# Kernel optimization log

Measured on AMD Instinct MI355X. Metric: run time of the kernel, lower is better.

## Reference

```python
import jax, jax.numpy as jnp
import numpy as np

T = 20000          # document length in tokens
EMBED_DIM = 300    # GloVe 840B.300d
STATE_DIM = 400    # 2 * lstm_dim (bidirectional)
HIDDEN = 150       # Scorer hidden_dim default
MAX_N = 10         # span widths 1..10
G_DIM = 2 * STATE_DIM + EMBED_DIM  # 1100


def _mlp3(x, W1, b1, W2, b2, W3, b3):
    # Scorer: Linear -> ReLU -> Linear -> ReLU -> Linear(->1)
    h = jax.nn.relu(x @ W1 + b1)
    h = jax.nn.relu(h @ W2 + b2)
    return h @ W3 + b3


def _span_features(embeds, states, attn_logits):
    """Vectorized SpanEncoder: for every window of width n in 1..MAX_N,
    softmax the per-token attention logits within the window, attention-pool
    the word embeddings, and concat [state_start, state_end, pooled].
    Returns g of shape [sum_n (T-n+1), G_DIM]."""
    gs = []
    for n in range(1, MAX_N + 1):
        S = T - n + 1  # number of width-n spans
        # [n, S] windowed logits and [n, S, E] windowed embeds via shifted slices
        a = jnp.stack([attn_logits[j:j + S] for j in range(n)], axis=0)
        w = jax.nn.softmax(a, axis=0)  # softmax within each span (dim=0 in torch)
        we = jnp.stack([embeds[j:j + S] for j in range(n)], axis=0)
        pooled = jnp.einsum('ns,nse->se', w, we)  # [S, E]
        g = jnp.concatenate([states[:S], states[n - 1:n - 1 + S], pooled], axis=-1)
        gs.append(g)
    return jnp.concatenate(gs, axis=0)


def setup_inputs() -> dict:
    key = jax.random.key(0)
    ks = jax.random.split(key, 16)
    sc = 0.05
    return {
        'embeds': jax.random.normal(ks[0], (T, EMBED_DIM), jnp.float32),
        'states': jax.random.normal(ks[1], (T, STATE_DIM), jnp.float32),
        'attn_W1': jax.random.normal(ks[2], (STATE_DIM, HIDDEN), jnp.float32) * sc,
        'attn_b1': jnp.zeros((HIDDEN,), jnp.float32),
        'attn_W2': jax.random.normal(ks[3], (HIDDEN, HIDDEN), jnp.float32) * sc,
        'attn_b2': jnp.zeros((HIDDEN,), jnp.float32),
        'attn_W3': jax.random.normal(ks[4], (HIDDEN, 1), jnp.float32) * sc,
        'attn_b3': jnp.zeros((1,), jnp.float32),
        'sc_W1': jax.random.normal(ks[5], (G_DIM, HIDDEN), jnp.float32) * sc,
        'sc_b1': jnp.zeros((HIDDEN,), jnp.float32),
        'sc_W2': jax.random.normal(ks[6], (HIDDEN, HIDDEN), jnp.float32) * sc,
        'sc_b2': jnp.zeros((HIDDEN,), jnp.float32),
        'sc_W3': jax.random.normal(ks[7], (HIDDEN, 1), jnp.float32) * sc,
        'sc_b3': jnp.zeros((1,), jnp.float32),
    }


def reference(embeds, states, attn_W1, attn_b1, attn_W2, attn_b2, attn_W3, attn_b3,
              sc_W1, sc_b1, sc_W2, sc_b2, sc_W3, sc_b3):
    # SpanAttention: per-token scalar attention logit from the BiLSTM state
    attn_logits = _mlp3(states, attn_W1, attn_b1, attn_W2, attn_b2, attn_W3, attn_b3)[:, 0]
    # SpanEncoder: ragged windowed attention pooling + boundary-state concat
    g = _span_features(embeds, states, attn_logits)  # [10T-45, 1100]
    # SpanScorer: MLP score per span
    scores = _mlp3(g, sc_W1, sc_b1, sc_W2, sc_b2, sc_W3, sc_b3)[:, 0]
    return scores
```

## Files before the change

### kernel.cpp

```cpp
#include <hip/hip_runtime.h>
#include <hip/hip_bf16.h>
#include <math.h>

#define T_LEN 20000
#define HID 150

typedef __attribute__((ext_vector_type(8))) __bf16 bf16x8;
typedef __attribute__((ext_vector_type(4))) float f32x4;

__device__ __forceinline__ short f2bf(float f) {
    unsigned u = __float_as_uint(f);
    u = (u + 0x7fff + ((u >> 16) & 1)) >> 16;
    return (short)u;
}

__device__ __forceinline__ unsigned pk2(float a, float b) {
    __hip_bfloat162 h = __float22bfloat162_rn(make_float2(a, b));
    return *(unsigned*)&h;
}

__device__ __forceinline__ bf16x8 cvt8(float4 a, float4 b) {
    union { unsigned u[4]; bf16x8 v; } r;
    r.u[0] = pk2(a.x, a.y);
    r.u[1] = pk2(a.z, a.w);
    r.u[2] = pk2(b.x, b.y);
    r.u[3] = pk2(b.z, b.w);
    return r.v;
}

__device__ __forceinline__ float2 ubf2(unsigned u) {
    return make_float2(__uint_as_float(u << 16),
                       __uint_as_float(u & 0xffff0000u));
}

__global__ __launch_bounds__(256) void wprep(
    const float* __restrict__ sc_W1, const float* __restrict__ attn_W1,
    const float* __restrict__ attn_W2, const float* __restrict__ sc_W2,
    short* __restrict__ frag)
{
    int t = blockIdx.x * 256 + threadIdx.x;
    if (t >= 302080) return;
    float v = 0.f;
    if (t < 199680) {
        int e = t & 7, g = t >> 3;
        int lane = g & 63, h = g >> 6;
        int ks = h % 13, nt = h / 13;
        int k = ks * 32 + (lane >> 4) * 8 + e;
        int cs = (nt % 10) * 16 + (lane & 15);
        if (k < 400 && cs < HID) {
            if (nt < 10)      v = sc_W1[(long)k * HID + cs];
            else if (nt < 20) v = sc_W1[(long)(400 + k) * HID + cs];
            else              v = attn_W1[(long)k * HID + cs];
        }
    } else if (t < 250880) {
        int r = t - 199680;
        int e = r & 7, g = r >> 3;
        int lane = g & 63, h = g >> 6;
        int ks = h % 10, nt = h / 10;
        int k = ks * 32 + (lane >> 4) * 8 + e;
        int cs = nt * 16 + (lane & 15);
        if (k < 300 && cs < HID) v = sc_W1[(long)(800 + k) * HID + cs];
    } else if (t < 276480) {
        int r = t - 250880;
        int e = r & 7, g = r >> 3;
        int lane = g & 63, h = g >> 6;
        int ks = h % 5, nt = h / 5;
        int k = ks * 32 + (lane >> 4) * 8 + e;
        int cs = nt * 16 + (lane & 15);
        if (k < HID && cs < HID) v = attn_W2[(long)k * HID + cs];
    } else {
        int r = t - 276480;
        int e = r & 7, g = r >> 3;
        int lane = g & 63, h = g >> 6;
        int ks = h % 5, nt = h / 5;
        int k = ks * 32 + (lane >> 4) * 8 + e;
        int cs = nt * 16 + (lane & 15);
        if (k < HID && cs < HID) v = sc_W2[(long)k * HID + cs];
    }
    frag[t] = f2bf(v);
}

template<int NT, int KS>
__device__ __forceinline__ void mm_tiles(
    const short* __restrict__ fb,
    const short* As,
    int w, int lane, f32x4* acc)
{
    #pragma unroll
    for (int ks = 0; ks < KS; ++ks) {
        bf16x8 af = *(const bf16x8*)&As[(ks * 64 + lane) * 8];
        bf16x8 bfr[NT];
        #pragma unroll
        for (int t = 0; t < NT; ++t)
            bfr[t] = *(const bf16x8*)&fb[((4 * t + w) * KS + ks) << 9];
        #pragma unroll
        for (int t = 0; t < NT; ++t)
            acc[t] = __builtin_amdgcn_mfma_f32_16x16x32_bf16(bfr[t], af, acc[t], 0, 0, 0);
    }
}

__global__ __launch_bounds__(256, 4) void fusedAP(
    const float* __restrict__ states, const float* __restrict__ embeds,
    const short* __restrict__ frag,
    const float* __restrict__ scb1, const float* __restrict__ ab1,
    const float* __restrict__ ab2, const float* __restrict__ aW3,
    const float* __restrict__ ab3,
    short* __restrict__ Ubf, short* __restrict__ Vbf, short* __restrict__ Pbf,
    float* __restrict__ logits)
{
    __shared__ short As[13 * 64 * 8];
    __shared__ short h1s[16 * 168];
    __shared__ float red[16][4];
    __shared__ float sb1[160], ab1s[160];
    const int tid = threadIdx.x;
    const int w = tid >> 6, lane = tid & 63;
    const int ml = lane & 15, kg = lane >> 4;
    const int m0 = blockIdx.x * 16;

    for (int t = tid; t < 160; t += 256) {
        sb1[t]  = (t < HID) ? scb1[t] : 0.f;
        ab1s[t] = (t < HID) ? ab1[t]  : 0.f;
    }
    for (int g = tid; g < 13 * 64; g += 256) {
        int ks = g >> 6, l2 = g & 63;
        int k = ks * 32 + ((l2 >> 4) << 3);
        const float* Ar = states + (long)(m0 + (l2 & 15)) * 400;
        float4 a0 = make_float4(0.f, 0.f, 0.f, 0.f), a1 = a0;
        if (k + 4 <= 400) a0 = *(const float4*)&Ar[k];
        if (k + 8 <= 400) a1 = *(const float4*)&Ar[k + 4];
        *(bf16x8*)&As[g * 8] = cvt8(a0, a1);
    }
    __syncthreads();

    f32x4 acc[8];
    #pragma unroll
    for (int t = 0; t < 8; ++t) acc[t] = (f32x4){0.f, 0.f, 0.f, 0.f};
    const short* fb = frag + lane * 8;
    if (w < 2) mm_tiles<8, 13>(fb, As, w, lane, acc);
    else       mm_tiles<7, 13>(fb, As, w, lane, acc);

    const int nT = (w < 2) ? 8 : 7;
    #pragma unroll
    for (int t = 0; t < 8; ++t) {
        if (t < nT) {
            int nt = 4 * t + w;
            if (nt < 10) {
                int col0 = nt * 16 + kg * 4;
                float v[4];
                #pragma unroll
                for (int r = 0; r < 4; ++r) {
                    int c = col0 + r;
                    v[r] = (c < HID) ? acc[t][r] + sb1[c] : 0.f;
                }
                *(uint2*)&Ubf[(long)(m0 + ml) * 160 + col0] =
                    make_uint2(pk2(v[0], v[1]), pk2(v[2], v[3]));
            } else if (nt < 20) {
                int col0 = (nt - 10) * 16 + kg * 4;
                float v[4];
                #pragma unroll
                for (int r = 0; r < 4; ++r) {
                    int c = col0 + r;
                    v[r] = (c < HID) ? acc[t][r] : 0.f;
                }
                *(uint2*)&Vbf[(long)(m0 + ml) * 160 + col0] =
                    make_uint2(pk2(v[0], v[1]), pk2(v[2], v[3]));
            } else {
                int col0 = (nt - 20) * 16 + kg * 4;
                float v[4];
                #pragma unroll
                for (int r = 0; r < 4; ++r) {
                    int c = col0 + r;
                    v[r] = (c < HID) ? fmaxf(acc[t][r] + ab1s[c], 0.f) : 0.f;
                }
                *(uint2*)&h1s[ml * 168 + col0] =
                    make_uint2(pk2(v[0], v[1]), pk2(v[2], v[3]));
            }
        }
    }
    __syncthreads();

    for (int g = tid; g < 10 * 64; g += 256) {
        int ks = g >> 6, l2 = g & 63;
        int k = ks * 32 + ((l2 >> 4) << 3);
        const float* Er = embeds + (long)(m0 + (l2 & 15)) * 300;
        float4 a0 = make_float4(0.f, 0.f, 0.f, 0.f), a1 = a0;
        if (k + 4 <= 300) a0 = *(const float4*)&Er[k];
        if (k + 8 <= 300) a1 = *(const float4*)&Er[k + 4];
        *(bf16x8*)&As[g * 8] = cvt8(a0, a1);
    }
    __syncthreads();

    {
        f32x4 accP[3];
        #pragma unroll
        for (int t = 0; t < 3; ++t) accP[t] = (f32x4){0.f, 0.f, 0.f, 0.f};
        const short* fP = frag + 199680 + lane * 8;
        if (w < 2) mm_tiles<3, 10>(fP, As, w, lane, accP);
        else       mm_tiles<2, 10>(fP, As, w, lane, accP);

        const int nTp = (w < 2) ? 3 : 2;
        #pragma unroll
        for (int t = 0; t < 3; ++t) {
            if (t < nTp) {
                int nt = 4 * t + w;
                int col0 = nt * 16 + kg * 4;
                float v[4];
                #pragma unroll
                for (int r = 0; r < 4; ++r) {
                    int c = col0 + r;
                    v[r] = (c < HID) ? accP[t][r] : 0.f;
                }
                *(uint2*)&Pbf[(long)(m0 + ml) * 160 + col0] =
                    make_uint2(pk2(v[0], v[1]), pk2(v[2], v[3]));
            }
        }
    }

    const short* fAt2 = frag + 250880 + lane * 8;
    bf16x8 af2[5];
    #pragma unroll
    for (int ks = 0; ks < 5; ++ks)
        af2[ks] = *(const bf16x8*)&h1s[ml * 168 + ks * 32 + kg * 8];

    const int nT2 = (w < 2) ? 3 : 2;
    float score[4] = {0.f, 0.f, 0.f, 0.f};
    #pragma unroll
    for (int t = 0; t < 3; ++t) {
        if (t < nT2) {
            int nt = 4 * t + w;
            bf16x8 wb[5];
            #pragma unroll
            for (int ks = 0; ks < 5; ++ks)
                wb[ks] = *(const bf16x8*)&fAt2[(nt * 5 + ks) << 9];
            f32x4 a2 = {0.f, 0.f, 0.f, 0.f};
            #pragma unroll
            for (int ks = 0; ks < 5; ++ks)
                a2 = __builtin_amdgcn_mfma_f32_16x16x32_bf16(af2[ks], wb[ks], a2, 0, 0, 0);
            int col = nt * 16 + ml;
            float b2v = (col < HID) ? ab2[col] : 0.f;
            float w3v = (col < HID) ? aW3[col] : 0.f;
            #pragma unroll
            for (int r = 0; r < 4; ++r)
                score[r] += fmaxf(a2[r] + b2v, 0.f) * w3v;
        }
    }
    #pragma unroll
    for (int r = 0; r < 4; ++r) {
        score[r] += __shfl_xor(score[r], 1);
        score[r] += __shfl_xor(score[r], 2);
        score[r] += __shfl_xor(score[r], 4);
        score[r] += __shfl_xor(score[r], 8);
    }
    if (ml == 0) {
        #pragma unroll
        for (int r = 0; r < 4; ++r) red[kg * 4 + r][w] = score[r];
    }
    __syncthreads();
    if (tid < 16)
        logits[m0 + tid] = red[tid][0] + red[tid][1] + red[tid][2] + red[tid][3] + ab3[0];
}

__global__ __launch_bounds__(256) void span_all(
    const short* __restrict__ Ubf, const short* __restrict__ Vbf,
    const short* __restrict__ Pbf, const float* __restrict__ logits,
    const short* __restrict__ fW2, const float* __restrict__ b2,
    const float* __restrict__ W3, const float* __restrict__ b3,
    float* __restrict__ out)
{
    __shared__ short h1s[2][32 * 168];
    __shared__ float red[2][32][2];
    __shared__ float Ls[48], ebuf[48];
    __shared__ float b2s[160], W3s[160];

    const int tid = threadIdx.x;
    const int s0 = blockIdx.x * 32;
    const int nlo = blockIdx.y ? 6 : 1;
    const int nhi = blockIdx.y ? 10 : 5;

    if (tid < 48) {
        int r = s0 + tid; if (r > T_LEN - 1) r = T_LEN - 1;
        Ls[tid] = (tid < 41) ? logits[r] : -1e30f;
    }
    for (int t = tid; t < 160; t += 256) {
        b2s[t] = (t < HID) ? b2[t] : 0.f;
        W3s[t] = (t < HID) ? W3[t] : 0.f;
    }
    __syncthreads();
    if (tid < 48) {
        float M = -1e30f;
        for (int t = 0; t < 41; ++t) M = fmaxf(M, Ls[t]);
        ebuf[tid] = (tid < 41) ? expf(Ls[tid] - M) : 0.f;
    }
    __syncthreads();

    const int i = tid >> 3;
    const int q = tid & 7;
    const int d0 = 20 * q;
    const int s = s0 + i;
    int su = s; if (su > T_LEN - 1) su = T_LEN - 1;

    float Ur[20];
    {
        const uint2* U2 = (const uint2*)&Ubf[(long)su * 160 + d0];
        #pragma unroll
        for (int c = 0; c < 5; ++c) {
            uint2 uv = U2[c];
            float2 a = ubf2(uv.x), b_ = ubf2(uv.y);
            Ur[4 * c + 0] = a.x;  Ur[4 * c + 1] = a.y;
            Ur[4 * c + 2] = b_.x; Ur[4 * c + 3] = b_.y;
        }
    }
    float accp[20];
    #pragma unroll
    for (int d = 0; d < 20; ++d) accp[d] = 0.f;
    float den = 0.f;

    for (int j = 0; j < nlo - 1; ++j) {
        int rr_ = s + j; if (rr_ > T_LEN - 1) rr_ = T_LEN - 1;
        float e = ebuf[i + j];
        den += e;
        const uint2* P2 = (const uint2*)&Pbf[(long)rr_ * 160 + d0];
        #pragma unroll
        for (int c = 0; c < 5; ++c) {
            uint2 pv = P2[c];
            float2 a = ubf2(pv.x), b_ = ubf2(pv.y);
            accp[4 * c + 0] += e * a.x;  accp[4 * c + 1] += e * a.y;
            accp[4 * c + 2] += e * b_.x; accp[4 * c + 3] += e * b_.y;
        }
    }

    const int w = tid >> 6, lane = tid & 63;
    const int ml = lane & 15, kg = lane >> 4;
    const int mt = w >> 1;
    const int nt0 = (w & 1) * 5;
    const float bb = b3[0];
    const short* fw = fW2 + ((nt0 * 5) << 9) + lane * 8;

    auto phase1 = [&](int n, int p) {
        int rr_ = s + n - 1; if (rr_ > T_LEN - 1) rr_ = T_LEN - 1;
        float e = ebuf[i + n - 1];
        den += e;
        {
            const uint2* P2 = (const uint2*)&Pbf[(long)rr_ * 160 + d0];
            #pragma unroll
            for (int c = 0; c < 5; ++c) {
                uint2 pv = P2[c];
                float2 a = ubf2(pv.x), b_ = ubf2(pv.y);
                accp[4 * c + 0] += e * a.x;  accp[4 * c + 1] += e * a.y;
                accp[4 * c + 2] += e * b_.x; accp[4 * c + 3] += e * b_.y;
            }
        }
        float invd = 1.f / den;
        {
            const uint2* V2 = (const uint2*)&Vbf[(long)rr_ * 160 + d0];
            #pragma unroll
            for (int c = 0; c < 5; ++c) {
                uint2 vv = V2[c];
                float2 a = ubf2(vv.x), b_ = ubf2(vv.y);
                float x0 = fmaxf(Ur[4 * c + 0] + a.x  + accp[4 * c + 0] * invd, 0.f);
                float x1 = fmaxf(Ur[4 * c + 1] + a.y  + accp[4 * c + 1] * invd, 0.f);
                float x2 = fmaxf(Ur[4 * c + 2] + b_.x + accp[4 * c + 2] * invd, 0.f);
                float x3 = fmaxf(Ur[4 * c + 3] + b_.y + accp[4 * c + 3] * invd, 0.f);
                *(uint2*)&h1s[p][i * 168 + d0 + 4 * c] =
                    make_uint2(pk2(x0, x1), pk2(x2, x3));
            }
        }
    };

    phase1(nlo, 0);
    __syncthreads();

    for (int n = nlo; n <= nhi; ++n) {
        const int p = (n - nlo) & 1;

        bf16x8 af[5];
        #pragma unroll
        for (int ks = 0; ks < 5; ++ks)
            af[ks] = *(const bf16x8*)&h1s[p][(mt * 16 + ml) * 168 + ks * 32 + kg * 8];

        if (n < nhi) phase1(n + 1, 1 - p);

        bf16x8 wc[5], wn[5];
        #pragma unroll
        for (int ks = 0; ks < 5; ++ks)
            wc[ks] = *(const bf16x8*)&fw[ks << 9];

        float sc[4] = {0.f, 0.f, 0.f, 0.f};
        #pragma unroll
        for (int j = 0; j < 5; ++j) {
            if (j < 4) {
                #pragma unroll
                for (int ks = 0; ks < 5; ++ks)
                    wn[ks] = *(const bf16x8*)&fw[((j + 1) * 5 + ks) << 9];
            }
            f32x4 a2 = {0.f, 0.f, 0.f, 0.f};
            #pragma unroll
            for (int ks = 0; ks < 5; ++ks)
                a2 = __builtin_amdgcn_mfma_f32_16x16x32_bf16(af[ks], wc[ks], a2, 0, 0, 0);
            int col = (nt0 + j) * 16 + ml;
            float b2v = b2s[col], w3v = W3s[col];
            #pragma unroll
            for (int r = 0; r < 4; ++r)
                sc[r] += fmaxf(a2[r] + b2v, 0.f) * w3v;
            #pragma unroll
            for (int ks = 0; ks < 5; ++ks) wc[ks] = wn[ks];
        }
        #pragma unroll
        for (int r = 0; r < 4; ++r) {
            sc[r] += __shfl_xor(sc[r], 1);
            sc[r] += __shfl_xor(sc[r], 2);
            sc[r] += __shfl_xor(sc[r], 4);
            sc[r] += __shfl_xor(sc[r], 8);
        }
        if (ml == 0) {
            #pragma unroll
            for (int r = 0; r < 4; ++r)
                red[p][mt * 16 + kg * 4 + r][w & 1] = sc[r];
        }
        __syncthreads();
        if (tid < 32) {
            int S = T_LEN - n + 1;
            int off = (n - 1) * (T_LEN + 1) - (n - 1) * n / 2;
            int sr = s0 + tid;
            if (sr < S) out[off + sr] = red[p][tid][0] + red[p][tid][1] + bb;
        }
    }
}

extern "C" void kernel_launch(void* const* d_in, const int* in_sizes, int n_in,
                              void* d_out, int out_size, void* d_ws, size_t ws_size,
                              hipStream_t stream) {
    const float* embeds  = (const float*)d_in[0];
    const float* states  = (const float*)d_in[1];
    const float* attn_W1 = (const float*)d_in[2];
    const float* attn_b1 = (const float*)d_in[3];
    const float* attn_W2 = (const float*)d_in[4];
    const float* attn_b2 = (const float*)d_in[5];
    const float* attn_W3 = (const float*)d_in[6];
    const float* attn_b3 = (const float*)d_in[7];
    const float* sc_W1   = (const float*)d_in[8];
    const float* sc_b1   = (const float*)d_in[9];
    const float* sc_W2   = (const float*)d_in[10];
    const float* sc_b2   = (const float*)d_in[11];
    const float* sc_W3   = (const float*)d_in[12];
    const float* sc_b3   = (const float*)d_in[13];
    float* out = (float*)d_out;

    short* wsS = (short*)d_ws;
    short* Ubf = wsS;
    short* Vbf = wsS + 3200256;
    short* Pbf = wsS + 6400512;
    short* frag = wsS + 9600768;
    float* logits = (float*)(wsS + 9902848);

    wprep<<<1180, 256, 0, stream>>>(sc_W1, attn_W1, attn_W2, sc_W2, frag);
    fusedAP<<<1250, 256, 0, stream>>>(states, embeds, frag, sc_b1, attn_b1,
                                      attn_b2, attn_W3, attn_b3,
                                      Ubf, Vbf, Pbf, logits);
    span_all<<<dim3(625, 2), 256, 0, stream>>>(Ubf, Vbf, Pbf, logits,
                                               frag + 276480, sc_b2, sc_W3, sc_b3,
                                               out);
}
```

Before: 191.6 us.

## Process two row tiles per block in fusedAP and restructure span_all weight loads

fusedAP now handles 32 rows per block with 6 warps, and each warp owns 5 contiguous column tiles. Each B-fragment load from global memory feeds two MFMAs (one per 16-row group), and the next k-step's weights are software-prefetched, which halves grid size and weight traffic per row. In span_all, phase1 for the next width now runs before the A-fragment reads, and the register double-buffered weight prefetch is replaced by direct per-MFMA global loads, which lowers register pressure but may expose load latency. Larger LDS and register use per block may lower occupancy.

```diff
diff --git a/kernel.cpp b/kernel.cpp
--- a/kernel.cpp
+++ b/kernel.cpp
@@ -80,26 +80,7 @@
     frag[t] = f2bf(v);
 }
 
-template<int NT, int KS>
-__device__ __forceinline__ void mm_tiles(
-    const short* __restrict__ fb,
-    const short* As,
-    int w, int lane, f32x4* acc)
-{
-    #pragma unroll
-    for (int ks = 0; ks < KS; ++ks) {
-        bf16x8 af = *(const bf16x8*)&As[(ks * 64 + lane) * 8];
-        bf16x8 bfr[NT];
-        #pragma unroll
-        for (int t = 0; t < NT; ++t)
-            bfr[t] = *(const bf16x8*)&fb[((4 * t + w) * KS + ks) << 9];
-        #pragma unroll
-        for (int t = 0; t < NT; ++t)
-            acc[t] = __builtin_amdgcn_mfma_f32_16x16x32_bf16(bfr[t], af, acc[t], 0, 0, 0);
-    }
-}
-
-__global__ __launch_bounds__(256, 4) void fusedAP(
+__global__ __launch_bounds__(384, 3) void fusedAP(
     const float* __restrict__ states, const float* __restrict__ embeds,
     const short* __restrict__ frag,
     const float* __restrict__ scb1, const float* __restrict__ ab1,
@@ -108,61 +89,88 @@
     short* __restrict__ Ubf, short* __restrict__ Vbf, short* __restrict__ Pbf,
     float* __restrict__ logits)
 {
-    __shared__ short As[13 * 64 * 8];
-    __shared__ short h1s[16 * 168];
-    __shared__ float red[16][4];
+    __shared__ short As[2 * 13 * 64 * 8];
+    __shared__ short h1s[32 * 168];
+    __shared__ float red[32][6];
     __shared__ float sb1[160], ab1s[160];
     const int tid = threadIdx.x;
     const int w = tid >> 6, lane = tid & 63;
     const int ml = lane & 15, kg = lane >> 4;
-    const int m0 = blockIdx.x * 16;
-
-    for (int t = tid; t < 160; t += 256) {
+    const int m0 = blockIdx.x * 32;
+
+    for (int t = tid; t < 160; t += 384) {
         sb1[t]  = (t < HID) ? scb1[t] : 0.f;
         ab1s[t] = (t < HID) ? ab1[t]  : 0.f;
     }
-    for (int g = tid; g < 13 * 64; g += 256) {
-        int ks = g >> 6, l2 = g & 63;
+    for (int idx = tid; idx < 2 * 13 * 64; idx += 384) {
+        int g = idx / 832, r = idx - g * 832;
+        int ks = r >> 6, l2 = r & 63;
         int k = ks * 32 + ((l2 >> 4) << 3);
-        const float* Ar = states + (long)(m0 + (l2 & 15)) * 400;
+        const float* Ar = states + (long)(m0 + g * 16 + (l2 & 15)) * 400;
         float4 a0 = make_float4(0.f, 0.f, 0.f, 0.f), a1 = a0;
         if (k + 4 <= 400) a0 = *(const float4*)&Ar[k];
         if (k + 8 <= 400) a1 = *(const float4*)&Ar[k + 4];
-        *(bf16x8*)&As[g * 8] = cvt8(a0, a1);
-    }
-    __syncthreads();
-
-    f32x4 acc[8];
-    #pragma unroll
-    for (int t = 0; t < 8; ++t) acc[t] = (f32x4){0.f, 0.f, 0.f, 0.f};
+        *(bf16x8*)&As[idx * 8] = cvt8(a0, a1);
+    }
+    __syncthreads();
+
+    f32x4 acc[5][2];
+    #pragma unroll
+    for (int t = 0; t < 5; ++t)
+        #pragma unroll
+        for (int g = 0; g < 2; ++g)
+            acc[t][g] = (f32x4){0.f, 0.f, 0.f, 0.f};
+
     const short* fb = frag + lane * 8;
-    if (w < 2) mm_tiles<8, 13>(fb, As, w, lane, acc);
-    else       mm_tiles<7, 13>(fb, As, w, lane, acc);
-
-    const int nT = (w < 2) ? 8 : 7;
-    #pragma unroll
-    for (int t = 0; t < 8; ++t) {
-        if (t < nT) {
-            int nt = 4 * t + w;
-            if (nt < 10) {
+    const int t5 = w * 5;
+
+    bf16x8 bcur[5], bnxt[5];
+    #pragma unroll
+    for (int t = 0; t < 5; ++t)
+        bcur[t] = *(const bf16x8*)&fb[((t5 + t) * 13 + 0) << 9];
+
+    #pragma unroll
+    for (int ks = 0; ks < 13; ++ks) {
+        if (ks < 12) {
+            #pragma unroll
+            for (int t = 0; t < 5; ++t)
+                bnxt[t] = *(const bf16x8*)&fb[((t5 + t) * 13 + ks + 1) << 9];
+        }
+        bf16x8 af0 = *(const bf16x8*)&As[(ks * 64 + lane) * 8];
+        bf16x8 af1 = *(const bf16x8*)&As[((832 + ks * 64) + lane) * 8];
+        #pragma unroll
+        for (int t = 0; t < 5; ++t) {
+            acc[t][0] = __builtin_amdgcn_mfma_f32_16x16x32_bf16(bcur[t], af0, acc[t][0], 0, 0, 0);
+            acc[t][1] = __builtin_amdgcn_mfma_f32_16x16x32_bf16(bcur[t], af1, acc[t][1], 0, 0, 0);
+        }
+        #pragma unroll
+        for (int t = 0; t < 5; ++t) bcur[t] = bnxt[t];
+    }
+
+    #pragma unroll
+    for (int t = 0; t < 5; ++t) {
+        int nt = t5 + t;
+        #pragma unroll
+        for (int g = 0; g < 2; ++g) {
+            if (w < 2) {
                 int col0 = nt * 16 + kg * 4;
                 float v[4];
                 #pragma unroll
                 for (int r = 0; r < 4; ++r) {
                     int c = col0 + r;
-                    v[r] = (c < HID) ? acc[t][r] + sb1[c] : 0.f;
+                    v[r] = (c < HID) ? acc[t][g][r] + sb1[c] : 0.f;
                 }
-                *(uint2*)&Ubf[(long)(m0 + ml) * 160 + col0] =
+                *(uint2*)&Ubf[(long)(m0 + g * 16 + ml) * 160 + col0] =
                     make_uint2(pk2(v[0], v[1]), pk2(v[2], v[3]));
-            } else if (nt < 20) {
+            } else if (w < 4) {
                 int col0 = (nt - 10) * 16 + kg * 4;
                 float v[4];
                 #pragma unroll
                 for (int r = 0; r < 4; ++r) {
                     int c = col0 + r;
-                    v[r] = (c < HID) ? acc[t][r] : 0.f;
+                    v[r] = (c < HID) ? acc[t][g][r] : 0.f;
                 }
-                *(uint2*)&Vbf[(long)(m0 + ml) * 160 + col0] =
+                *(uint2*)&Vbf[(long)(m0 + g * 16 + ml) * 160 + col0] =
                     make_uint2(pk2(v[0], v[1]), pk2(v[2], v[3]));
             } else {
                 int col0 = (nt - 20) * 16 + kg * 4;
@@ -170,94 +178,142 @@
                 #pragma unroll
                 for (int r = 0; r < 4; ++r) {
                     int c = col0 + r;
-                    v[r] = (c < HID) ? fmaxf(acc[t][r] + ab1s[c], 0.f) : 0.f;
+                    v[r] = (c < HID) ? fmaxf(acc[t][g][r] + ab1s[c], 0.f) : 0.f;
                 }
-                *(uint2*)&h1s[ml * 168 + col0] =
+                *(uint2*)&h1s[(g * 16 + ml) * 168 + col0] =
                     make_uint2(pk2(v[0], v[1]), pk2(v[2], v[3]));
             }
         }
     }
     __syncthreads();
 
-    for (int g = tid; g < 10 * 64; g += 256) {
-        int ks = g >> 6, l2 = g & 63;
+    for (int idx = tid; idx < 2 * 10 * 64; idx += 384) {
+        int g = idx / 640, r = idx - g * 640;
+        int ks = r >> 6, l2 = r & 63;
         int k = ks * 32 + ((l2 >> 4) << 3);
-        const float* Er = embeds + (long)(m0 + (l2 & 15)) * 300;
+        const float* Er = embeds + (long)(m0 + g * 16 + (l2 & 15)) * 300;
         float4 a0 = make_float4(0.f, 0.f, 0.f, 0.f), a1 = a0;
         if (k + 4 <= 300) a0 = *(const float4*)&Er[k];
         if (k + 8 <= 300) a1 = *(const float4*)&Er[k + 4];
-        *(bf16x8*)&As[g * 8] = cvt8(a0, a1);
-    }
-    __syncthreads();
-
+        *(bf16x8*)&As[idx * 8] = cvt8(a0, a1);
+    }
+    __syncthreads();
+
+    const int tB = (w < 4) ? 2 * w : (w == 4 ? 8 : 9);
+    const int nTP = (w < 4) ? 2 : 1;
     {
-        f32x4 accP[3];
-        #pragma unroll
-        for (int t = 0; t < 3; ++t) accP[t] = (f32x4){0.f, 0.f, 0.f, 0.f};
+        f32x4 accP[2][2];
+        #pragma unroll
+        for (int t = 0; t < 2; ++t)
+            #pragma unroll
+            for (int g = 0; g < 2; ++g)
+                accP[t][g] = (f32x4){0.f, 0.f, 0.f, 0.f};
+
         const short* fP = frag + 199680 + lane * 8;
-        if (w < 2) mm_tiles<3, 10>(fP, As, w, lane, accP);
-        else       mm_tiles<2, 10>(fP, As, w, lane, accP);
-
-        const int nTp = (w < 2) ? 3 : 2;
-        #pragma unroll
-        for (int t = 0; t < 3; ++t) {
-            if (t < nTp) {
-                int nt = 4 * t + w;
-                int col0 = nt * 16 + kg * 4;
-                float v[4];
-                #pragma unroll
-                for (int r = 0; r < 4; ++r) {
-                    int c = col0 + r;
-                    v[r] = (c < HID) ? accP[t][r] : 0.f;
+        bf16x8 pcur[2], pnxt[2];
+        #pragma unroll
+        for (int t = 0; t < 2; ++t)
+            if (t < nTP) pcur[t] = *(const bf16x8*)&fP[((tB + t) * 10 + 0) << 9];
+
+        #pragma unroll
+        for (int ks = 0; ks < 10; ++ks) {
+            if (ks < 9) {
+                #pragma unroll
+                for (int t = 0; t < 2; ++t)
+                    if (t < nTP) pnxt[t] = *(const bf16x8*)&fP[((tB + t) * 10 + ks + 1) << 9];
+            }
+            bf16x8 af0 = *(const bf16x8*)&As[(ks * 64 + lane) * 8];
+            bf16x8 af1 = *(const bf16x8*)&As[((640 + ks * 64) + lane) * 8];
+            #pragma unroll
+            for (int t = 0; t < 2; ++t) {
+                if (t < nTP) {
+                    accP[t][0] = __builtin_amdgcn_mfma_f32_16x16x32_bf16(pcur[t], af0, accP[t][0], 0, 0, 0);
+                    accP[t][1] = __builtin_amdgcn_mfma_f32_16x16x32_bf16(pcur[t], af1, accP[t][1], 0, 0, 0);
                 }
-                *(uint2*)&Pbf[(long)(m0 + ml) * 160 + col0] =
-                    make_uint2(pk2(v[0], v[1]), pk2(v[2], v[3]));
+            }
+            #pragma unroll
+            for (int t = 0; t < 2; ++t) pcur[t] = pnxt[t];
+        }
+
+        #pragma unroll
+        for (int t = 0; t < 2; ++t) {
+            if (t < nTP) {
+                int col0 = (tB + t) * 16 + kg * 4;
+                #pragma unroll
+                for (int g = 0; g < 2; ++g) {
+                    float v[4];
+                    #pragma unroll
+                    for (int r = 0; r < 4; ++r) {
+                        int c = col0 + r;
+                        v[r] = (c < HID) ? accP[t][g][r] : 0.f;
+                    }
+                    *(uint2*)&Pbf[(long)(m0 + g * 16 + ml) * 160 + col0] =
+                        make_uint2(pk2(v[0], v[1]), pk2(v[2], v[3]));
+                }
             }
         }
     }
 
     const short* fAt2 = frag + 250880 + lane * 8;
-    bf16x8 af2[5];
-    #pragma unroll
-    for (int ks = 0; ks < 5; ++ks)
-        af2[ks] = *(const bf16x8*)&h1s[ml * 168 + ks * 32 + kg * 8];
-
-    const int nT2 = (w < 2) ? 3 : 2;
-    float score[4] = {0.f, 0.f, 0.f, 0.f};
-    #pragma unroll
-    for (int t = 0; t < 3; ++t) {
-        if (t < nT2) {
-            int nt = 4 * t + w;
+    bf16x8 af2[2][5];
+    #pragma unroll
+    for (int g = 0; g < 2; ++g)
+        #pragma unroll
+        for (int ks = 0; ks < 5; ++ks)
+            af2[g][ks] = *(const bf16x8*)&h1s[(g * 16 + ml) * 168 + ks * 32 + kg * 8];
+
+    float score[2][4];
+    #pragma unroll
+    for (int g = 0; g < 2; ++g)
+        #pragma unroll
+        for (int r = 0; r < 4; ++r) score[g][r] = 0.f;
+
+    #pragma unroll
+    for (int t = 0; t < 2; ++t) {
+        if (t < nTP) {
+            int nt = tB + t;
             bf16x8 wb[5];
             #pragma unroll
             for (int ks = 0; ks < 5; ++ks)
                 wb[ks] = *(const bf16x8*)&fAt2[(nt * 5 + ks) << 9];
-            f32x4 a2 = {0.f, 0.f, 0.f, 0.f};
-            #pragma unroll
-            for (int ks = 0; ks < 5; ++ks)
-                a2 = __builtin_amdgcn_mfma_f32_16x16x32_bf16(af2[ks], wb[ks], a2, 0, 0, 0);
+            f32x4 a2[2];
+            a2[0] = (f32x4){0.f, 0.f, 0.f, 0.f};
+            a2[1] = (f32x4){0.f, 0.f, 0.f, 0.f};
+            #pragma unroll
+            for (int g = 0; g < 2; ++g)
+                #pragma unroll
+                for (int ks = 0; ks < 5; ++ks)
+                    a2[g] = __builtin_amdgcn_mfma_f32_16x16x32_bf16(af2[g][ks], wb[ks], a2[g], 0, 0, 0);
             int col = nt * 16 + ml;
             float b2v = (col < HID) ? ab2[col] : 0.f;
             float w3v = (col < HID) ? aW3[col] : 0.f;
             #pragma unroll
+            for (int g = 0; g < 2; ++g)
+                #pragma unroll
+                for (int r = 0; r < 4; ++r)
+                    score[g][r] += fmaxf(a2[g][r] + b2v, 0.f) * w3v;
+        }
+    }
+    #pragma unroll
+    for (int g = 0; g < 2; ++g)
+        #pragma unroll
+        for (int r = 0; r < 4; ++r) {
+            score[g][r] += __shfl_xor(score[g][r], 1);
+            score[g][r] += __shfl_xor(score[g][r], 2);
+            score[g][r] += __shfl_xor(score[g][r], 4);
+            score[g][r] += __shfl_xor(score[g][r], 8);
+        }
+    if (ml == 0) {
+        #pragma unroll
+        for (int g = 0; g < 2; ++g)
+            #pragma unroll
             for (int r = 0; r < 4; ++r)
-                score[r] += fmaxf(a2[r] + b2v, 0.f) * w3v;
-        }
-    }
-    #pragma unroll
-    for (int r = 0; r < 4; ++r) {
-        score[r] += __shfl_xor(score[r], 1);
-        score[r] += __shfl_xor(score[r], 2);
-        score[r] += __shfl_xor(score[r], 4);
-        score[r] += __shfl_xor(score[r], 8);
-    }
-    if (ml == 0) {
-        #pragma unroll
-        for (int r = 0; r < 4; ++r) red[kg * 4 + r][w] = score[r];
-    }
-    __syncthreads();
-    if (tid < 16)
-        logits[m0 + tid] = red[tid][0] + red[tid][1] + red[tid][2] + red[tid][3] + ab3[0];
+                red[g * 16 + kg * 4 + r][w] = score[g][r];
+    }
+    __syncthreads();
+    if (tid < 32)
+        logits[m0 + tid] = red[tid][0] + red[tid][1] + red[tid][2] +
+                           red[tid][3] + red[tid][4] + red[tid][5] + ab3[0];
 }
 
 __global__ __launch_bounds__(256) void span_all(
@@ -334,7 +390,6 @@
     const int mt = w >> 1;
     const int nt0 = (w & 1) * 5;
     const float bb = b3[0];
-    const short* fw = fW2 + ((nt0 * 5) << 9) + lane * 8;
 
     auto phase1 = [&](int n, int p) {
         int rr_ = s + n - 1; if (rr_ > T_LEN - 1) rr_ = T_LEN - 1;
@@ -372,38 +427,28 @@
 
     for (int n = nlo; n <= nhi; ++n) {
         const int p = (n - nlo) & 1;
+        if (n < nhi) phase1(n + 1, 1 - p);
 
         bf16x8 af[5];
         #pragma unroll
         for (int ks = 0; ks < 5; ++ks)
             af[ks] = *(const bf16x8*)&h1s[p][(mt * 16 + ml) * 168 + ks * 32 + kg * 8];
 
-        if (n < nhi) phase1(n + 1, 1 - p);
-
-        bf16x8 wc[5], wn[5];
-        #pragma unroll
-        for (int ks = 0; ks < 5; ++ks)
-            wc[ks] = *(const bf16x8*)&fw[ks << 9];
-
         float sc[4] = {0.f, 0.f, 0.f, 0.f};
         #pragma unroll
         for (int j = 0; j < 5; ++j) {
-            if (j < 4) {
-                #pragma unroll
-                for (int ks = 0; ks < 5; ++ks)
-                    wn[ks] = *(const bf16x8*)&fw[((j + 1) * 5 + ks) << 9];
-            }
+            int nt = nt0 + j;
             f32x4 a2 = {0.f, 0.f, 0.f, 0.f};
             #pragma unroll
-            for (int ks = 0; ks < 5; ++ks)
-                a2 = __builtin_amdgcn_mfma_f32_16x16x32_bf16(af[ks], wc[ks], a2, 0, 0, 0);
-            int col = (nt0 + j) * 16 + ml;
+            for (int ks = 0; ks < 5; ++ks) {
+                bf16x8 bf = *(const bf16x8*)&fW2[(long)(((nt * 5 + ks) << 6) | lane) << 3];
+                a2 = __builtin_amdgcn_mfma_f32_16x16x32_bf16(af[ks], bf, a2, 0, 0, 0);
+            }
+            int col = nt * 16 + ml;
             float b2v = b2s[col], w3v = W3s[col];
             #pragma unroll
             for (int r = 0; r < 4; ++r)
                 sc[r] += fmaxf(a2[r] + b2v, 0.f) * w3v;
-            #pragma unroll
-            for (int ks = 0; ks < 5; ++ks) wc[ks] = wn[ks];
         }
         #pragma unroll
         for (int r = 0; r < 4; ++r) {
@@ -454,9 +499,9 @@
     float* logits = (float*)(wsS + 9902848);
 
     wprep<<<1180, 256, 0, stream>>>(sc_W1, attn_W1, attn_W2, sc_W2, frag);
-    fusedAP<<<1250, 256, 0, stream>>>(states, embeds, frag, sc_b1, attn_b1,
-                                      attn_b2, attn_W3, attn_b3,
-                                      Ubf, Vbf, Pbf, logits);
+    fusedAP<<<625, 384, 0, stream>>>(states, embeds, frag, sc_b1, attn_b1,
+                                     attn_b2, attn_W3, attn_b3,
+                                     Ubf, Vbf, Pbf, logits);
     span_all<<<dim3(625, 2), 256, 0, stream>>>(Ubf, Vbf, Pbf, logits,
                                                frag + 276480, sc_b2, sc_W3, sc_b3,
                                                out);
```

Result: slower. 199.9 us (+4.4%).

## Split fused projection kernel across grid y and spread span widths over more blocks

Applied to the files above, without the earlier changes.

The fused projection kernel now launches a 2D grid. The y=0 blocks compute the U/V boundary projections and the y=1 blocks compute the attention MLP, the pooled-embedding projection and the logits, so each block holds fewer accumulator tiles and more blocks run at once. The span scorer grid goes from 2 to 5 width groups of two widths each, which adds parallelism at the cost of reloading states more often. The explicit weight-fragment double-buffering in the span loop is replaced by direct per-tile loads, and the next-width phase1 is now issued before the fragment reads. The occupancy hint of 4 on fusedAP is dropped, and the staging of states into LDS is duplicated across both y blocks.

```diff
diff --git a/kernel.cpp b/kernel.cpp
--- a/kernel.cpp
+++ b/kernel.cpp
@@ -80,26 +80,7 @@
     frag[t] = f2bf(v);
 }
 
-template<int NT, int KS>
-__device__ __forceinline__ void mm_tiles(
-    const short* __restrict__ fb,
-    const short* As,
-    int w, int lane, f32x4* acc)
-{
-    #pragma unroll
-    for (int ks = 0; ks < KS; ++ks) {
-        bf16x8 af = *(const bf16x8*)&As[(ks * 64 + lane) * 8];
-        bf16x8 bfr[NT];
-        #pragma unroll
-        for (int t = 0; t < NT; ++t)
-            bfr[t] = *(const bf16x8*)&fb[((4 * t + w) * KS + ks) << 9];
-        #pragma unroll
-        for (int t = 0; t < NT; ++t)
-            acc[t] = __builtin_amdgcn_mfma_f32_16x16x32_bf16(bfr[t], af, acc[t], 0, 0, 0);
-    }
-}
-
-__global__ __launch_bounds__(256, 4) void fusedAP(
+__global__ __launch_bounds__(256) void fusedAP(
     const float* __restrict__ states, const float* __restrict__ embeds,
     const short* __restrict__ frag,
     const float* __restrict__ scb1, const float* __restrict__ ab1,
@@ -132,19 +113,30 @@
     }
     __syncthreads();
 
-    f32x4 acc[8];
-    #pragma unroll
-    for (int t = 0; t < 8; ++t) acc[t] = (f32x4){0.f, 0.f, 0.f, 0.f};
     const short* fb = frag + lane * 8;
-    if (w < 2) mm_tiles<8, 13>(fb, As, w, lane, acc);
-    else       mm_tiles<7, 13>(fb, As, w, lane, acc);
-
-    const int nT = (w < 2) ? 8 : 7;
-    #pragma unroll
-    for (int t = 0; t < 8; ++t) {
-        if (t < nT) {
-            int nt = 4 * t + w;
-            if (nt < 10) {
+
+    if (blockIdx.y == 0) {
+        const int t5 = w * 5;
+        f32x4 acc[5];
+        #pragma unroll
+        for (int t = 0; t < 5; ++t) acc[t] = (f32x4){0.f, 0.f, 0.f, 0.f};
+
+        #pragma unroll
+        for (int ks = 0; ks < 13; ++ks) {
+            bf16x8 af = *(const bf16x8*)&As[(ks * 64 + lane) * 8];
+            bf16x8 bfr[5];
+            #pragma unroll
+            for (int t = 0; t < 5; ++t)
+                bfr[t] = *(const bf16x8*)&fb[((t5 + t) * 13 + ks) << 9];
+            #pragma unroll
+            for (int t = 0; t < 5; ++t)
+                acc[t] = __builtin_amdgcn_mfma_f32_16x16x32_bf16(bfr[t], af, acc[t], 0, 0, 0);
+        }
+
+        #pragma unroll
+        for (int t = 0; t < 5; ++t) {
+            int nt = t5 + t;
+            if (w < 2) {
                 int col0 = nt * 16 + kg * 4;
                 float v[4];
                 #pragma unroll
@@ -154,7 +146,7 @@
                 }
                 *(uint2*)&Ubf[(long)(m0 + ml) * 160 + col0] =
                     make_uint2(pk2(v[0], v[1]), pk2(v[2], v[3]));
-            } else if (nt < 20) {
+            } else {
                 int col0 = (nt - 10) * 16 + kg * 4;
                 float v[4];
                 #pragma unroll
@@ -164,8 +156,37 @@
                 }
                 *(uint2*)&Vbf[(long)(m0 + ml) * 160 + col0] =
                     make_uint2(pk2(v[0], v[1]), pk2(v[2], v[3]));
-            } else {
-                int col0 = (nt - 20) * 16 + kg * 4;
+            }
+        }
+        return;
+    }
+
+    const int nT = (w < 2) ? 3 : 2;
+    const int t0 = (w < 2) ? 3 * w : 6 + 2 * (w - 2);
+
+    {
+        f32x4 acc[3];
+        #pragma unroll
+        for (int t = 0; t < 3; ++t) acc[t] = (f32x4){0.f, 0.f, 0.f, 0.f};
+
+        #pragma unroll
+        for (int ks = 0; ks < 13; ++ks) {
+            bf16x8 af = *(const bf16x8*)&As[(ks * 64 + lane) * 8];
+            bf16x8 bfr[3];
+            #pragma unroll
+            for (int t = 0; t < 3; ++t)
+                if (t < nT)
+                    bfr[t] = *(const bf16x8*)&fb[((20 + t0 + t) * 13 + ks) << 9];
+            #pragma unroll
+            for (int t = 0; t < 3; ++t)
+                if (t < nT)
+                    acc[t] = __builtin_amdgcn_mfma_f32_16x16x32_bf16(bfr[t], af, acc[t], 0, 0, 0);
+        }
+
+        #pragma unroll
+        for (int t = 0; t < 3; ++t) {
+            if (t < nT) {
+                int col0 = (t0 + t) * 16 + kg * 4;
                 float v[4];
                 #pragma unroll
                 for (int r = 0; r < 4; ++r) {
@@ -188,22 +209,73 @@
         if (k + 8 <= 300) a1 = *(const float4*)&Er[k + 4];
         *(bf16x8*)&As[g * 8] = cvt8(a0, a1);
     }
-    __syncthreads();
 
     {
+        const short* fAt2 = frag + 250880 + lane * 8;
+        bf16x8 af2[5];
+        #pragma unroll
+        for (int ks = 0; ks < 5; ++ks)
+            af2[ks] = *(const bf16x8*)&h1s[ml * 168 + ks * 32 + kg * 8];
+
+        float score[4] = {0.f, 0.f, 0.f, 0.f};
+        #pragma unroll
+        for (int t = 0; t < 3; ++t) {
+            if (t < nT) {
+                int nt = t0 + t;
+                bf16x8 wb[5];
+                #pragma unroll
+                for (int ks = 0; ks < 5; ++ks)
+                    wb[ks] = *(const bf16x8*)&fAt2[(nt * 5 + ks) << 9];
+                f32x4 a2 = {0.f, 0.f, 0.f, 0.f};
+                #pragma unroll
+                for (int ks = 0; ks < 5; ++ks)
+                    a2 = __builtin_amdgcn_mfma_f32_16x16x32_bf16(af2[ks], wb[ks], a2, 0, 0, 0);
+                int col = nt * 16 + ml;
+                float b2v = (col < HID) ? ab2[col] : 0.f;
+                float w3v = (col < HID) ? aW3[col] : 0.f;
+                #pragma unroll
+                for (int r = 0; r < 4; ++r)
+                    score[r] += fmaxf(a2[r] + b2v, 0.f) * w3v;
+            }
+        }
+        #pragma unroll
+        for (int r = 0; r < 4; ++r) {
+            score[r] += __shfl_xor(score[r], 1);
+            score[r] += __shfl_xor(score[r], 2);
+            score[r] += __shfl_xor(score[r], 4);
+            score[r] += __shfl_xor(score[r], 8);
+        }
+        if (ml == 0) {
+            #pragma unroll
+            for (int r = 0; r < 4; ++r) red[kg * 4 + r][w] = score[r];
+        }
+    }
+    __syncthreads();
+
+    {
+        const short* fP = frag + 199680 + lane * 8;
         f32x4 accP[3];
         #pragma unroll
         for (int t = 0; t < 3; ++t) accP[t] = (f32x4){0.f, 0.f, 0.f, 0.f};
-        const short* fP = frag + 199680 + lane * 8;
-        if (w < 2) mm_tiles<3, 10>(fP, As, w, lane, accP);
-        else       mm_tiles<2, 10>(fP, As, w, lane, accP);
-
-        const int nTp = (w < 2) ? 3 : 2;
+
+        #pragma unroll
+        for (int ks = 0; ks < 10; ++ks) {
+            bf16x8 af = *(const bf16x8*)&As[(ks * 64 + lane) * 8];
+            bf16x8 bfr[3];
+            #pragma unroll
+            for (int t = 0; t < 3; ++t)
+                if (t < nT)
+                    bfr[t] = *(const bf16x8*)&fP[((t0 + t) * 10 + ks) << 9];
+            #pragma unroll
+            for (int t = 0; t < 3; ++t)
+                if (t < nT)
+                    accP[t] = __builtin_amdgcn_mfma_f32_16x16x32_bf16(bfr[t], af, accP[t], 0, 0, 0);
+        }
+
         #pragma unroll
         for (int t = 0; t < 3; ++t) {
-            if (t < nTp) {
-                int nt = 4 * t + w;
-                int col0 = nt * 16 + kg * 4;
+            if (t < nT) {
+                int col0 = (t0 + t) * 16 + kg * 4;
                 float v[4];
                 #pragma unroll
                 for (int r = 0; r < 4; ++r) {
@@ -216,46 +288,6 @@
         }
     }
 
-    const short* fAt2 = frag + 250880 + lane * 8;
-    bf16x8 af2[5];
-    #pragma unroll
-    for (int ks = 0; ks < 5; ++ks)
-        af2[ks] = *(const bf16x8*)&h1s[ml * 168 + ks * 32 + kg * 8];
-
-    const int nT2 = (w < 2) ? 3 : 2;
-    float score[4] = {0.f, 0.f, 0.f, 0.f};
-    #pragma unroll
-    for (int t = 0; t < 3; ++t) {
-        if (t < nT2) {
-            int nt = 4 * t + w;
-            bf16x8 wb[5];
-            #pragma unroll
-            for (int ks = 0; ks < 5; ++ks)
-                wb[ks] = *(const bf16x8*)&fAt2[(nt * 5 + ks) << 9];
-            f32x4 a2 = {0.f, 0.f, 0.f, 0.f};
-            #pragma unroll
-            for (int ks = 0; ks < 5; ++ks)
-                a2 = __builtin_amdgcn_mfma_f32_16x16x32_bf16(af2[ks], wb[ks], a2, 0, 0, 0);
-            int col = nt * 16 + ml;
-            float b2v = (col < HID) ? ab2[col] : 0.f;
-            float w3v = (col < HID) ? aW3[col] : 0.f;
-            #pragma unroll
-            for (int r = 0; r < 4; ++r)
-                score[r] += fmaxf(a2[r] + b2v, 0.f) * w3v;
-        }
-    }
-    #pragma unroll
-    for (int r = 0; r < 4; ++r) {
-        score[r] += __shfl_xor(score[r], 1);
-        score[r] += __shfl_xor(score[r], 2);
-        score[r] += __shfl_xor(score[r], 4);
-        score[r] += __shfl_xor(score[r], 8);
-    }
-    if (ml == 0) {
-        #pragma unroll
-        for (int r = 0; r < 4; ++r) red[kg * 4 + r][w] = score[r];
-    }
-    __syncthreads();
     if (tid < 16)
         logits[m0 + tid] = red[tid][0] + red[tid][1] + red[tid][2] + red[tid][3] + ab3[0];
 }
@@ -274,8 +306,8 @@
 
     const int tid = threadIdx.x;
     const int s0 = blockIdx.x * 32;
-    const int nlo = blockIdx.y ? 6 : 1;
-    const int nhi = blockIdx.y ? 10 : 5;
+    const int nlo = 2 * blockIdx.y + 1;
+    const int nhi = nlo + 1;
 
     if (tid < 48) {
         int r = s0 + tid; if (r > T_LEN - 1) r = T_LEN - 1;
@@ -334,7 +366,6 @@
     const int mt = w >> 1;
     const int nt0 = (w & 1) * 5;
     const float bb = b3[0];
-    const short* fw = fW2 + ((nt0 * 5) << 9) + lane * 8;
 
     auto phase1 = [&](int n, int p) {
         int rr_ = s + n - 1; if (rr_ > T_LEN - 1) rr_ = T_LEN - 1;
@@ -372,38 +403,28 @@
 
     for (int n = nlo; n <= nhi; ++n) {
         const int p = (n - nlo) & 1;
+        if (n < nhi) phase1(n + 1, 1 - p);
 
         bf16x8 af[5];
         #pragma unroll
         for (int ks = 0; ks < 5; ++ks)
             af[ks] = *(const bf16x8*)&h1s[p][(mt * 16 + ml) * 168 + ks * 32 + kg * 8];
 
-        if (n < nhi) phase1(n + 1, 1 - p);
-
-        bf16x8 wc[5], wn[5];
-        #pragma unroll
-        for (int ks = 0; ks < 5; ++ks)
-            wc[ks] = *(const bf16x8*)&fw[ks << 9];
-
         float sc[4] = {0.f, 0.f, 0.f, 0.f};
         #pragma unroll
         for (int j = 0; j < 5; ++j) {
-            if (j < 4) {
-                #pragma unroll
-                for (int ks = 0; ks < 5; ++ks)
-                    wn[ks] = *(const bf16x8*)&fw[((j + 1) * 5 + ks) << 9];
-            }
+            int nt = nt0 + j;
             f32x4 a2 = {0.f, 0.f, 0.f, 0.f};
             #pragma unroll
-            for (int ks = 0; ks < 5; ++ks)
-                a2 = __builtin_amdgcn_mfma_f32_16x16x32_bf16(af[ks], wc[ks], a2, 0, 0, 0);
-            int col = (nt0 + j) * 16 + ml;
+            for (int ks = 0; ks < 5; ++ks) {
+                bf16x8 bf = *(const bf16x8*)&fW2[(long)(((nt * 5 + ks) << 6) | lane) << 3];
+                a2 = __builtin_amdgcn_mfma_f32_16x16x32_bf16(af[ks], bf, a2, 0, 0, 0);
+            }
+            int col = nt * 16 + ml;
             float b2v = b2s[col], w3v = W3s[col];
             #pragma unroll
             for (int r = 0; r < 4; ++r)
                 sc[r] += fmaxf(a2[r] + b2v, 0.f) * w3v;
-            #pragma unroll
-            for (int ks = 0; ks < 5; ++ks) wc[ks] = wn[ks];
         }
         #pragma unroll
         for (int r = 0; r < 4; ++r) {
@@ -454,10 +475,10 @@
     float* logits = (float*)(wsS + 9902848);
 
     wprep<<<1180, 256, 0, stream>>>(sc_W1, attn_W1, attn_W2, sc_W2, frag);
-    fusedAP<<<1250, 256, 0, stream>>>(states, embeds, frag, sc_b1, attn_b1,
-                                      attn_b2, attn_W3, attn_b3,
-                                      Ubf, Vbf, Pbf, logits);
-    span_all<<<dim3(625, 2), 256, 0, stream>>>(Ubf, Vbf, Pbf, logits,
+    fusedAP<<<dim3(1250, 2), 256, 0, stream>>>(states, embeds, frag, sc_b1, attn_b1,
+                                               attn_b2, attn_W3, attn_b3,
+                                               Ubf, Vbf, Pbf, logits);
+    span_all<<<dim3(625, 5), 256, 0, stream>>>(Ubf, Vbf, Pbf, logits,
                                                frag + 276480, sc_b2, sc_W3, sc_b3,
                                                out);
 }
```

After: 203.2 us. 6.1% more time.

## Use prefix sums for windowed attention pooling in span scoring kernel

Applied to the files above, without the earlier changes.

Rewrites span_all so that each block of 16 span starts first builds per-dimension prefix sums of exp-weighted projected embeddings, plus a prefix sum of the exp weights, in shared memory. Any window's pooled term then comes from two prefix-sum differences rather than incremental accumulation. The span widths are split across the four waves. Each wave builds its MFMA A fragments straight from registers and writes scores without a shared-memory reduction or barriers. The trade-offs are a serial 25-step prefix scan per block, every wave loading all ten W2 tiles, and strided shared-memory reads of the Cs table.

```diff
diff --git a/kernel.cpp b/kernel.cpp
--- a/kernel.cpp
+++ b/kernel.cpp
@@ -31,6 +31,10 @@
 __device__ __forceinline__ float2 ubf2(unsigned u) {
     return make_float2(__uint_as_float(u << 16),
                        __uint_as_float(u & 0xffff0000u));
+}
+
+__device__ __forceinline__ float bf2f(short s) {
+    return __uint_as_float(((unsigned)(unsigned short)s) << 16);
 }
 
 __global__ __launch_bounds__(256) void wprep(
@@ -267,143 +271,109 @@
     const float* __restrict__ W3, const float* __restrict__ b3,
     float* __restrict__ out)
 {
-    __shared__ short h1s[2][32 * 168];
-    __shared__ float red[2][32][2];
-    __shared__ float Ls[48], ebuf[48];
+    __shared__ float Cs[160][29];
+    __shared__ float Es[32];
+    __shared__ float Ls[32];
     __shared__ float b2s[160], W3s[160];
 
     const int tid = threadIdx.x;
-    const int s0 = blockIdx.x * 32;
-    const int nlo = blockIdx.y ? 6 : 1;
-    const int nhi = blockIdx.y ? 10 : 5;
-
-    if (tid < 48) {
+    const int s0 = blockIdx.x * 16;
+
+    if (tid < 32) {
         int r = s0 + tid; if (r > T_LEN - 1) r = T_LEN - 1;
-        Ls[tid] = (tid < 41) ? logits[r] : -1e30f;
+        Ls[tid] = (tid < 25) ? logits[r] : -1e30f;
     }
     for (int t = tid; t < 160; t += 256) {
         b2s[t] = (t < HID) ? b2[t] : 0.f;
         W3s[t] = (t < HID) ? W3[t] : 0.f;
     }
     __syncthreads();
-    if (tid < 48) {
+
+    if (tid < 160) {
         float M = -1e30f;
-        for (int t = 0; t < 41; ++t) M = fmaxf(M, Ls[t]);
-        ebuf[tid] = (tid < 41) ? expf(Ls[tid] - M) : 0.f;
-    }
-    __syncthreads();
-
-    const int i = tid >> 3;
-    const int q = tid & 7;
-    const int d0 = 20 * q;
-    const int s = s0 + i;
-    int su = s; if (su > T_LEN - 1) su = T_LEN - 1;
-
-    float Ur[20];
-    {
-        const uint2* U2 = (const uint2*)&Ubf[(long)su * 160 + d0];
-        #pragma unroll
-        for (int c = 0; c < 5; ++c) {
-            uint2 uv = U2[c];
-            float2 a = ubf2(uv.x), b_ = ubf2(uv.y);
-            Ur[4 * c + 0] = a.x;  Ur[4 * c + 1] = a.y;
-            Ur[4 * c + 2] = b_.x; Ur[4 * c + 3] = b_.y;
-        }
-    }
-    float accp[20];
-    #pragma unroll
-    for (int d = 0; d < 20; ++d) accp[d] = 0.f;
-    float den = 0.f;
-
-    for (int j = 0; j < nlo - 1; ++j) {
-        int rr_ = s + j; if (rr_ > T_LEN - 1) rr_ = T_LEN - 1;
-        float e = ebuf[i + j];
-        den += e;
-        const uint2* P2 = (const uint2*)&Pbf[(long)rr_ * 160 + d0];
-        #pragma unroll
-        for (int c = 0; c < 5; ++c) {
-            uint2 pv = P2[c];
-            float2 a = ubf2(pv.x), b_ = ubf2(pv.y);
-            accp[4 * c + 0] += e * a.x;  accp[4 * c + 1] += e * a.y;
-            accp[4 * c + 2] += e * b_.x; accp[4 * c + 3] += e * b_.y;
-        }
-    }
+        #pragma unroll
+        for (int t = 0; t < 25; ++t) M = fmaxf(M, Ls[t]);
+        float c = 0.f;
+        Cs[tid][0] = 0.f;
+        #pragma unroll
+        for (int t = 0; t < 25; ++t) {
+            int r = s0 + t; if (r > T_LEN - 1) r = T_LEN - 1;
+            float e = expf(Ls[t] - M);
+            c += e * bf2f(Pbf[(long)r * 160 + tid]);
+            Cs[tid][t + 1] = c;
+        }
+    } else if (tid == 160) {
+        float M = -1e30f;
+        #pragma unroll
+        for (int t = 0; t < 25; ++t) M = fmaxf(M, Ls[t]);
+        float Ea = 0.f;
+        Es[0] = 0.f;
+        #pragma unroll
+        for (int t = 0; t < 25; ++t) { Ea += expf(Ls[t] - M); Es[t + 1] = Ea; }
+    }
+    __syncthreads();
 
     const int w = tid >> 6, lane = tid & 63;
     const int ml = lane & 15, kg = lane >> 4;
-    const int mt = w >> 1;
-    const int nt0 = (w & 1) * 5;
+    const int i = ml;
+    const int sr = s0 + i;
+    const int sru = (sr > T_LEN - 1) ? T_LEN - 1 : sr;
     const float bb = b3[0];
-    const short* fw = fW2 + ((nt0 * 5) << 9) + lane * 8;
-
-    auto phase1 = [&](int n, int p) {
-        int rr_ = s + n - 1; if (rr_ > T_LEN - 1) rr_ = T_LEN - 1;
-        float e = ebuf[i + n - 1];
-        den += e;
-        {
-            const uint2* P2 = (const uint2*)&Pbf[(long)rr_ * 160 + d0];
-            #pragma unroll
-            for (int c = 0; c < 5; ++c) {
-                uint2 pv = P2[c];
-                float2 a = ubf2(pv.x), b_ = ubf2(pv.y);
-                accp[4 * c + 0] += e * a.x;  accp[4 * c + 1] += e * a.y;
-                accp[4 * c + 2] += e * b_.x; accp[4 * c + 3] += e * b_.y;
+    const int nbeg = (w < 2) ? 3 * w + 1 : 2 * w + 3;
+    const int ncnt = (w < 2) ? 3 : 2;
+    const int d0 = kg * 8;
+
+    bf16x8 uf[5];
+    {
+        const short* Up = Ubf + (long)sru * 160 + d0;
+        #pragma unroll
+        for (int ks = 0; ks < 5; ++ks)
+            uf[ks] = *(const bf16x8*)&Up[ks * 32];
+    }
+    const float E0 = Es[i];
+    const short* fw = fW2 + lane * 8;
+
+    for (int nn = 0; nn < ncnt; ++nn) {
+        const int n = nbeg + nn;
+        const int j = i + n - 1;
+        int vr = s0 + j; if (vr > T_LEN - 1) vr = T_LEN - 1;
+        const float invd = 1.f / (Es[i + n] - E0);
+        const short* Vp = Vbf + (long)vr * 160 + d0;
+
+        bf16x8 af[5];
+        #pragma unroll
+        for (int ks = 0; ks < 5; ++ks) {
+            union { bf16x8 v; unsigned u[4]; } U_, V_, R_;
+            U_.v = uf[ks];
+            V_.v = *(const bf16x8*)&Vp[ks * 32];
+            #pragma unroll
+            for (int h = 0; h < 4; ++h) {
+                float2 ua = ubf2(U_.u[h]);
+                float2 va = ubf2(V_.u[h]);
+                int d = d0 + ks * 32 + 2 * h;
+                float p0 = (Cs[d][i + n]     - Cs[d][i])     * invd;
+                float p1 = (Cs[d + 1][i + n] - Cs[d + 1][i]) * invd;
+                float x0 = fmaxf(ua.x + va.x + p0, 0.f);
+                float x1 = fmaxf(ua.y + va.y + p1, 0.f);
+                R_.u[h] = pk2(x0, x1);
             }
-        }
-        float invd = 1.f / den;
-        {
-            const uint2* V2 = (const uint2*)&Vbf[(long)rr_ * 160 + d0];
-            #pragma unroll
-            for (int c = 0; c < 5; ++c) {
-                uint2 vv = V2[c];
-                float2 a = ubf2(vv.x), b_ = ubf2(vv.y);
-                float x0 = fmaxf(Ur[4 * c + 0] + a.x  + accp[4 * c + 0] * invd, 0.f);
-                float x1 = fmaxf(Ur[4 * c + 1] + a.y  + accp[4 * c + 1] * invd, 0.f);
-                float x2 = fmaxf(Ur[4 * c + 2] + b_.x + accp[4 * c + 2] * invd, 0.f);
-                float x3 = fmaxf(Ur[4 * c + 3] + b_.y + accp[4 * c + 3] * invd, 0.f);
-                *(uint2*)&h1s[p][i * 168 + d0 + 4 * c] =
-                    make_uint2(pk2(x0, x1), pk2(x2, x3));
+            af[ks] = R_.v;
+        }
+
+        float sc[4] = {0.f, 0.f, 0.f, 0.f};
+        #pragma unroll
+        for (int nt = 0; nt < 10; ++nt) {
+            f32x4 a2 = {0.f, 0.f, 0.f, 0.f};
+            #pragma unroll
+            for (int ks = 0; ks < 5; ++ks) {
+                bf16x8 bf = *(const bf16x8*)&fw[(nt * 5 + ks) << 9];
+                a2 = __builtin_amdgcn_mfma_f32_16x16x32_bf16(af[ks], bf, a2, 0, 0, 0);
             }
-        }
-    };
-
-    phase1(nlo, 0);
-    __syncthreads();
-
-    for (int n = nlo; n <= nhi; ++n) {
-        const int p = (n - nlo) & 1;
-
-        bf16x8 af[5];
-        #pragma unroll
-        for (int ks = 0; ks < 5; ++ks)
-            af[ks] = *(const bf16x8*)&h1s[p][(mt * 16 + ml) * 168 + ks * 32 + kg * 8];
-
-        if (n < nhi) phase1(n + 1, 1 - p);
-
-        bf16x8 wc[5], wn[5];
-        #pragma unroll
-        for (int ks = 0; ks < 5; ++ks)
-            wc[ks] = *(const bf16x8*)&fw[ks << 9];
-
-        float sc[4] = {0.f, 0.f, 0.f, 0.f};
-        #pragma unroll
-        for (int j = 0; j < 5; ++j) {
-            if (j < 4) {
-                #pragma unroll
-                for (int ks = 0; ks < 5; ++ks)
-                    wn[ks] = *(const bf16x8*)&fw[((j + 1) * 5 + ks) << 9];
-            }
-            f32x4 a2 = {0.f, 0.f, 0.f, 0.f};
-            #pragma unroll
-            for (int ks = 0; ks < 5; ++ks)
-                a2 = __builtin_amdgcn_mfma_f32_16x16x32_bf16(af[ks], wc[ks], a2, 0, 0, 0);
-            int col = (nt0 + j) * 16 + ml;
+            int col = nt * 16 + ml;
             float b2v = b2s[col], w3v = W3s[col];
             #pragma unroll
             for (int r = 0; r < 4; ++r)
                 sc[r] += fmaxf(a2[r] + b2v, 0.f) * w3v;
-            #pragma unroll
-            for (int ks = 0; ks < 5; ++ks) wc[ks] = wn[ks];
         }
         #pragma unroll
         for (int r = 0; r < 4; ++r) {
@@ -413,16 +383,12 @@
             sc[r] += __shfl_xor(sc[r], 8);
         }
         if (ml == 0) {
-            #pragma unroll
-            for (int r = 0; r < 4; ++r)
-                red[p][mt * 16 + kg * 4 + r][w & 1] = sc[r];
-        }
-        __syncthreads();
-        if (tid < 32) {
             int S = T_LEN - n + 1;
             int off = (n - 1) * (T_LEN + 1) - (n - 1) * n / 2;
-            int sr = s0 + tid;
-            if (sr < S) out[off + sr] = red[p][tid][0] + red[p][tid][1] + bb;
+            int so = s0 + kg * 4;
+            #pragma unroll
+            for (int r = 0; r < 4; ++r)
+                if (so + r < S) out[off + so + r] = sc[r] + bb;
         }
     }
 }
@@ -457,7 +423,7 @@
     fusedAP<<<1250, 256, 0, stream>>>(states, embeds, frag, sc_b1, attn_b1,
                                       attn_b2, attn_W3, attn_b3,
                                       Ubf, Vbf, Pbf, logits);
-    span_all<<<dim3(625, 2), 256, 0, stream>>>(Ubf, Vbf, Pbf, logits,
-                                               frag + 276480, sc_b2, sc_W3, sc_b3,
-                                               out);
-}
+    span_all<<<1250, 256, 0, stream>>>(Ubf, Vbf, Pbf, logits,
+                                       frag + 276480, sc_b2, sc_W3, sc_b3,
+                                       out);
+}
```

Measured after the change: 229.8 us. 1.2x slower.
